# Kernel tuning notes

Measured on AMD Instinct MI355X. Metric: run time of the kernel, lower is better.

## Reference

```python
import jax, jax.numpy as jnp
import numpy as np

TEMPERATURE = 0.07


def setup_inputs() -> dict:
    key = jax.random.key(0)
    k1, k2 = jax.random.split(key)
    B, V, C, H, W = 4, 2, 128, 32, 32
    features = jax.random.normal(k1, (B, V, C, H, W), dtype=jnp.float32)
    # L2-normalize per-pixel feature vectors (channel dim), as contrastive
    # embeddings are in practice; the original exp() is unstabilized.
    features = features / jnp.linalg.norm(features, axis=2, keepdims=True)
    labels = jax.random.randint(k2, (B, V, H, W), 0, 4, dtype=jnp.int32)
    return {"features": features, "labels": labels}


def reference(features, labels):
    B, V, C, H, W = features.shape
    # torch.cat(torch.unbind(features, dim=1), dim=0): views stacked along batch
    cf = jnp.transpose(features, (1, 0, 2, 3, 4)).reshape(B * V, C, H, W)
    # kernels = cf.permute(0,2,3,1).reshape(-1, C, 1, 1); conv2d with 1x1 kernels
    # == pairwise dot products of per-pixel feature vectors.
    X = jnp.transpose(cf, (0, 2, 3, 1)).reshape(-1, C)  # [N, C], N = B*V*H*W
    N = X.shape[0]
    logits = (X @ X.T) / TEMPERATURE  # [N, N]

    lab = jnp.transpose(labels, (1, 0, 2, 3)).reshape(-1)  # [N]
    mask = (lab[:, None] == lab[None, :]).astype(logits.dtype)  # [N, N]
    logits_mask = 1.0 - jnp.eye(N, dtype=logits.dtype)  # zero the diagonal
    mask = mask * logits_mask

    exp_logits = jnp.exp(logits) * logits_mask
    log_prob = logits - jnp.log(jnp.sum(exp_logits, axis=1, keepdims=True))
    mean_log_prob_pos = jnp.sum(mask * log_prob, axis=1) / jnp.sum(mask, axis=1)
    loss = -mean_log_prob_pos  # [N]

    non_bg = (lab != 0).astype(logits.dtype)
    return jnp.sum(loss * non_bg) / jnp.sum(non_bg)
```

## Files before the change

### kernel.cpp

```cpp
#include <hip/hip_runtime.h>
#include <hip/hip_bf16.h>
#include <stdint.h>

typedef short bf16x8 __attribute__((ext_vector_type(8)));
typedef float f32x16 __attribute__((ext_vector_type(16)));

#define NROWS 8192
#define CDIM  128
#define TEMP  0.07f
#define C1F   20.6099291555566248f

#define OFF_S    0
#define OFF_G    32768
#define OFF_HIST (32768 + 2048)
#define OFF_SUM  (32768 + 2048 + 16)
#define OFF_TKT  (32768 + 2048 + 16 + 4)
#define ZBYTES   (32768 + 2048 + 16 + 4 + 4)
#define ZWORDS   (ZBYTES / 4)

__device__ __forceinline__ float bf2f(unsigned short u) {
  union { unsigned int i; float f; } x; x.i = ((unsigned int)u) << 16; return x.f;
}
__device__ __forceinline__ unsigned short f2bf(float f) {
  union { float f; unsigned int i; } x; x.f = f;
  unsigned int r = x.i + 0x7fffu + ((x.i >> 16) & 1u);
  return (unsigned short)(r >> 16);
}
__device__ __forceinline__ float fexp2(float x) {
#if __has_builtin(__builtin_amdgcn_exp2f)
  return __builtin_amdgcn_exp2f(x);
#else
  return exp2f(x);
#endif
}

__global__ __launch_bounds__(256) void k_pack(const float* __restrict__ F,
                                              unsigned short* __restrict__ Xb,
                                              float* __restrict__ zbase) {
  const int tid = threadIdx.x;
  {
    int idx = blockIdx.x * 256 + tid;
    if (idx < ZWORDS) zbase[idx] = 0.0f;
  }
  __shared__ float lds[128 * 33];
  const int g   = blockIdx.x >> 5;
  const int hw0 = (blockIdx.x & 31) << 5;
#pragma unroll
  for (int p = 0; p < 16; ++p) {
    int c  = p * 8 + (tid >> 5);
    int hw = hw0 + (tid & 31);
    lds[c * 33 + (tid & 31)] = F[(g * 128 + c) * 1024 + hw];
  }
  __syncthreads();
#pragma unroll
  for (int p = 0; p < 16; ++p) {
    int hwl = p * 2 + (tid >> 7);
    int c   = tid & 127;
    int row = g * 1024 + hw0 + hwl;
    Xb[row * 128 + c] = f2bf(lds[c * 33 + hwl]);
  }
}

__global__ __launch_bounds__(256, 4) void k_main(const unsigned short* __restrict__ Xb,
                                                 const int* __restrict__ labels,
                                                 float* __restrict__ S,
                                                 float* __restrict__ G,
                                                 int* __restrict__ hist) {
  __shared__ int4 ldsB[2][2][16 * 33];
  const int bid = blockIdx.x;
  const int tid = threadIdx.x;
  const int lane = tid & 63;

  if (bid < 128) {
    const int rchunk = bid >> 3;
    const int cbase  = (bid & 7) * 16;
    const int cl     = tid & 15;
    const int rg     = tid >> 4;
    float a0 = 0.f, a1 = 0.f, a2 = 0.f, a3 = 0.f;
    const int nend = rchunk * 512 + 512;
    for (int n = rchunk * 512 + rg; n < nend; n += 16) {
      int   lab = labels[n];
      float v   = bf2f(Xb[n * 128 + cbase + cl]);
      a0 += (lab == 0) ? v : 0.f;
      a1 += (lab == 1) ? v : 0.f;
      a2 += (lab == 2) ? v : 0.f;
      a3 += (lab == 3) ? v : 0.f;
    }
    a0 += __shfl_xor(a0, 16, 64); a0 += __shfl_xor(a0, 32, 64);
    a1 += __shfl_xor(a1, 16, 64); a1 += __shfl_xor(a1, 32, 64);
    a2 += __shfl_xor(a2, 16, 64); a2 += __shfl_xor(a2, 32, 64);
    a3 += __shfl_xor(a3, 16, 64); a3 += __shfl_xor(a3, 32, 64);
    if (lane < 16) {
      int c = cbase + lane;
      atomicAdd(&G[0 * 128 + c], a0);
      atomicAdd(&G[1 * 128 + c], a1);
      atomicAdd(&G[2 * 128 + c], a2);
      atomicAdd(&G[3 * 128 + c], a3);
    }
    if (bid == 0) {
      int h0 = 0, h1 = 0, h2 = 0, h3 = 0;
      for (int n = tid; n < NROWS; n += 256) {
        int lab = labels[n];
        h0 += (lab == 0); h1 += (lab == 1); h2 += (lab == 2); h3 += (lab == 3);
      }
      for (int mm = 1; mm < 64; mm <<= 1) {
        h0 += __shfl_xor(h0, mm, 64); h1 += __shfl_xor(h1, mm, 64);
        h2 += __shfl_xor(h2, mm, 64); h3 += __shfl_xor(h3, mm, 64);
      }
      if (lane == 0) {
        atomicAdd(&hist[0], h0); atomicAdd(&hist[1], h1);
        atomicAdd(&hist[2], h2); atomicAdd(&hist[3], h3);
      }
    }
    return;
  }

  const int b        = bid - 128;
  const int wave     = tid >> 6;
  const int rowBlock = b >> 4;
  const int split    = b & 15;
  const int r0       = rowBlock * 128 + wave * 32;
  const int col0     = split * 512;
  const int m        = lane & 31;
  const int half     = lane >> 5;

  bf16x8 afrag[8];
#pragma unroll
  for (int s = 0; s < 8; ++s)
    afrag[s] = *(const bf16x8*)(Xb + (r0 + m) * CDIM + (half + 2 * s) * 8);

  float accS[16];
#pragma unroll
  for (int r = 0; r < 16; ++r) accS[r] = 0.f;

  const int n_l = tid >> 3;
  const int bq  = tid & 7;
  const unsigned short* src = Xb + (col0 + n_l) * CDIM + bq * 16;
  int4 v0 = *(const int4*)src;
  int4 v1 = *(const int4*)(src + 8);
  int4 v2 = *(const int4*)(src + 32 * CDIM);
  int4 v3 = *(const int4*)(src + 32 * CDIM + 8);
  ldsB[0][0][(2 * bq) * 33 + n_l]     = v0;
  ldsB[0][0][(2 * bq + 1) * 33 + n_l] = v1;
  ldsB[0][1][(2 * bq) * 33 + n_l]     = v2;
  ldsB[0][1][(2 * bq + 1) * 33 + n_l] = v3;
  src += 64 * CDIM;
  v0 = *(const int4*)src;
  v1 = *(const int4*)(src + 8);
  v2 = *(const int4*)(src + 32 * CDIM);
  v3 = *(const int4*)(src + 32 * CDIM + 8);

  for (int t = 0; t < 8; ++t) {
    __syncthreads();
    if (t < 7) {
      const int nb = (t + 1) & 1;
      ldsB[nb][0][(2 * bq) * 33 + n_l]     = v0;
      ldsB[nb][0][(2 * bq + 1) * 33 + n_l] = v1;
      ldsB[nb][1][(2 * bq) * 33 + n_l]     = v2;
      ldsB[nb][1][(2 * bq + 1) * 33 + n_l] = v3;
    }
    if (t < 6) {
      src += 64 * CDIM;
      v0 = *(const int4*)src;
      v1 = *(const int4*)(src + 8);
      v2 = *(const int4*)(src + 32 * CDIM);
      v3 = *(const int4*)(src + 32 * CDIM + 8);
    }
    const int cur = t & 1;
#pragma unroll
    for (int u = 0; u < 2; ++u) {
      f32x16 acc;
#pragma unroll
      for (int r = 0; r < 16; ++r) acc[r] = 0.f;
#pragma unroll
      for (int s = 0; s < 8; ++s) {
        bf16x8 bfrag = *(const bf16x8*)&ldsB[cur][u][(half + 2 * s) * 33 + m];
        acc = __builtin_amdgcn_mfma_f32_32x32x16_bf16(afrag[s], bfrag, acc, 0, 0, 0);
      }
      const int colbase = col0 + t * 64 + u * 32;
      if (r0 == colbase) {
        const int colg = colbase + m;
#pragma unroll
        for (int r = 0; r < 16; ++r) {
          int   row = r0 + (r & 3) + 8 * (r >> 2) + 4 * half;
          float arg = (row == colg) ? -1e30f : acc[r] * C1F;
          accS[r] += fexp2(arg);
        }
      } else {
#pragma unroll
        for (int r = 0; r < 16; ++r) accS[r] += fexp2(acc[r] * C1F);
      }
    }
  }

#pragma unroll
  for (int r = 0; r < 16; ++r) {
    float v = accS[r];
    v += __shfl_xor(v, 1, 64);
    v += __shfl_xor(v, 2, 64);
    v += __shfl_xor(v, 4, 64);
    v += __shfl_xor(v, 8, 64);
    v += __shfl_xor(v, 16, 64);
    accS[r] = v;
  }
  if (m == 0) {
#pragma unroll
    for (int r = 0; r < 16; ++r) {
      int row = r0 + (r & 3) + 8 * (r >> 2) + 4 * half;
      atomicAdd(&S[row], accS[r]);
    }
  }
}

__global__ __launch_bounds__(256) void k_loss(const unsigned short* __restrict__ Xb,
                                              const int* __restrict__ labels,
                                              const float* __restrict__ S,
                                              const float* __restrict__ G,
                                              const int* __restrict__ hist,
                                              float* __restrict__ sumLoss,
                                              int* __restrict__ ticket,
                                              float* __restrict__ out) {
  const int i   = blockIdx.x * 256 + threadIdx.x;
  const int lab = labels[i];
  const float* g = G + lab * 128;
  const unsigned short* x = Xb + i * CDIM;
  float dot = 0.f, nrm = 0.f;
#pragma unroll
  for (int cc = 0; cc < 16; ++cc) {
    int4 q = *(const int4*)(x + cc * 8);
    const unsigned int* qs = (const unsigned int*)&q;
#pragma unroll
    for (int j = 0; j < 4; ++j) {
      unsigned int u = qs[j];
      float lo = __uint_as_float(u << 16);
      float hi = __uint_as_float(u & 0xffff0000u);
      int   ci = cc * 8 + j * 2;
      dot += lo * g[ci] + hi * g[ci + 1];
      nrm += lo * lo + hi * hi;
    }
  }
  float Si   = S[i];
  float cnt  = (float)(hist[lab] - 1);
  float loss = logf(Si) - (dot - nrm) / (TEMP * cnt);
  float contrib = (lab != 0) ? loss : 0.f;
  for (int mm = 1; mm < 64; mm <<= 1) contrib += __shfl_xor(contrib, mm, 64);
  __shared__ float ws4[4];
  if ((threadIdx.x & 63) == 0) ws4[threadIdx.x >> 6] = contrib;
  __syncthreads();
  if (threadIdx.x == 0) {
    atomicAdd(sumLoss, ws4[0] + ws4[1] + ws4[2] + ws4[3]);
    __threadfence();
    int t = atomicAdd(ticket, 1);
    if (t == 31) {
      float total = atomicAdd(sumLoss, 0.0f);
      out[0] = total / (float)(NROWS - hist[0]);
    }
  }
}

extern "C" void kernel_launch(void* const* d_in, const int* in_sizes, int n_in,
                              void* d_out, int out_size, void* d_ws, size_t ws_size,
                              hipStream_t stream) {
  const float* F      = (const float*)d_in[0];
  const int*   labels = (const int*)d_in[1];
  char* ws = (char*)d_ws;

  unsigned short* Xb      = (unsigned short*)ws;
  const size_t    offS    = (size_t)NROWS * CDIM * 2;
  float*          S       = (float*)(ws + offS + OFF_S);
  float*          G       = (float*)(ws + offS + OFF_G);
  int*            hist    = (int*)(ws + offS + OFF_HIST);
  float*          sumLoss = (float*)(ws + offS + OFF_SUM);
  int*            ticket  = (int*)(ws + offS + OFF_TKT);

  hipLaunchKernelGGL(k_pack, dim3(256), dim3(256), 0, stream, F, Xb, S);
  hipLaunchKernelGGL(k_main, dim3(1152), dim3(256), 0, stream, Xb, labels, S, G, hist);
  hipLaunchKernelGGL(k_loss, dim3(32), dim3(256), 0, stream, Xb, labels, S, G, hist,
                     sumLoss, ticket, (float*)d_out);
}
```

Measured before the change: 100.4 us.

## Double rows per wave in logsumexp GEMM and move class sums into pack

Each wave now computes two 32-row MFMA tiles against every LDS-staged B fragment, so each block covers 256 rows and the grid drops from 1152 to 520 blocks. This halves B-tile loads and LDS traffic per output. The per-class feature sums and label histogram are computed as per-block partials inside the pack kernel from the fp32 LDS tile, then reduced by 8 extra blocks in the main kernel instead of 128 atomic-heavy blocks. The cost is higher register pressure (launch bounds lowered to 2 blocks per SM) and fewer blocks, which reduces parallelism and latency hiding.

```diff
diff --git a/kernel.cpp b/kernel.cpp
--- a/kernel.cpp
+++ b/kernel.cpp
@@ -17,6 +17,8 @@
 #define OFF_TKT  (32768 + 2048 + 16 + 4)
 #define ZBYTES   (32768 + 2048 + 16 + 4 + 4)
 #define ZWORDS   (ZBYTES / 4)
+#define OFF_GPART (ZBYTES + 8)
+#define OFF_CPART (OFF_GPART + 256 * 512 * 4)
 
 __device__ __forceinline__ float bf2f(unsigned short u) {
   union { unsigned int i; float f; } x; x.i = ((unsigned int)u) << 16; return x.f;
@@ -35,16 +37,22 @@
 }
 
 __global__ __launch_bounds__(256) void k_pack(const float* __restrict__ F,
+                                              const int* __restrict__ labels,
                                               unsigned short* __restrict__ Xb,
-                                              float* __restrict__ zbase) {
+                                              float* __restrict__ zbase,
+                                              float* __restrict__ Gpart,
+                                              int* __restrict__ Cpart) {
   const int tid = threadIdx.x;
   {
     int idx = blockIdx.x * 256 + tid;
     if (idx < ZWORDS) zbase[idx] = 0.0f;
   }
   __shared__ float lds[128 * 33];
+  __shared__ int   slab[32];
+  __shared__ float gred[4][128];
   const int g   = blockIdx.x >> 5;
   const int hw0 = (blockIdx.x & 31) << 5;
+  if (tid < 32) slab[tid] = labels[g * 1024 + hw0 + tid];
 #pragma unroll
   for (int p = 0; p < 16; ++p) {
     int c  = p * 8 + (tid >> 5);
@@ -59,79 +67,93 @@
     int row = g * 1024 + hw0 + hwl;
     Xb[row * 128 + c] = f2bf(lds[c * 33 + hwl]);
   }
-}
-
-__global__ __launch_bounds__(256, 4) void k_main(const unsigned short* __restrict__ Xb,
-                                                 const int* __restrict__ labels,
+  const int c  = tid & 127;
+  const int rh = tid >> 7;
+  float a0 = 0.f, a1 = 0.f, a2 = 0.f, a3 = 0.f;
+#pragma unroll
+  for (int k = 0; k < 16; ++k) {
+    int   hwl = rh * 16 + k;
+    float v   = lds[c * 33 + hwl];
+    int   lab = slab[hwl];
+    a0 += (lab == 0) ? v : 0.f;
+    a1 += (lab == 1) ? v : 0.f;
+    a2 += (lab == 2) ? v : 0.f;
+    a3 += (lab == 3) ? v : 0.f;
+  }
+  if (rh == 1) { gred[0][c] = a0; gred[1][c] = a1; gred[2][c] = a2; gred[3][c] = a3; }
+  if (tid >= 32 && tid < 36) {
+    int j = tid - 32, cnt = 0;
+#pragma unroll
+    for (int k2 = 0; k2 < 32; ++k2) cnt += (slab[k2] == j);
+    Cpart[blockIdx.x * 4 + j] = cnt;
+  }
+  __syncthreads();
+  if (rh == 0) {
+    float* gp = Gpart + blockIdx.x * 512;
+    gp[0 * 128 + c] = a0 + gred[0][c];
+    gp[1 * 128 + c] = a1 + gred[1][c];
+    gp[2 * 128 + c] = a2 + gred[2][c];
+    gp[3 * 128 + c] = a3 + gred[3][c];
+  }
+}
+
+__global__ __launch_bounds__(256, 2) void k_main(const unsigned short* __restrict__ Xb,
                                                  float* __restrict__ S,
                                                  float* __restrict__ G,
-                                                 int* __restrict__ hist) {
+                                                 int* __restrict__ hist,
+                                                 const float* __restrict__ Gpart,
+                                                 const int* __restrict__ Cpart) {
   __shared__ int4 ldsB[2][2][16 * 33];
-  const int bid = blockIdx.x;
-  const int tid = threadIdx.x;
+  const int bid  = blockIdx.x;
+  const int tid  = threadIdx.x;
   const int lane = tid & 63;
 
-  if (bid < 128) {
-    const int rchunk = bid >> 3;
-    const int cbase  = (bid & 7) * 16;
-    const int cl     = tid & 15;
-    const int rg     = tid >> 4;
-    float a0 = 0.f, a1 = 0.f, a2 = 0.f, a3 = 0.f;
-    const int nend = rchunk * 512 + 512;
-    for (int n = rchunk * 512 + rg; n < nend; n += 16) {
-      int   lab = labels[n];
-      float v   = bf2f(Xb[n * 128 + cbase + cl]);
-      a0 += (lab == 0) ? v : 0.f;
-      a1 += (lab == 1) ? v : 0.f;
-      a2 += (lab == 2) ? v : 0.f;
-      a3 += (lab == 3) ? v : 0.f;
-    }
-    a0 += __shfl_xor(a0, 16, 64); a0 += __shfl_xor(a0, 32, 64);
-    a1 += __shfl_xor(a1, 16, 64); a1 += __shfl_xor(a1, 32, 64);
-    a2 += __shfl_xor(a2, 16, 64); a2 += __shfl_xor(a2, 32, 64);
-    a3 += __shfl_xor(a3, 16, 64); a3 += __shfl_xor(a3, 32, 64);
-    if (lane < 16) {
-      int c = cbase + lane;
-      atomicAdd(&G[0 * 128 + c], a0);
-      atomicAdd(&G[1 * 128 + c], a1);
-      atomicAdd(&G[2 * 128 + c], a2);
-      atomicAdd(&G[3 * 128 + c], a3);
-    }
-    if (bid == 0) {
-      int h0 = 0, h1 = 0, h2 = 0, h3 = 0;
-      for (int n = tid; n < NROWS; n += 256) {
-        int lab = labels[n];
-        h0 += (lab == 0); h1 += (lab == 1); h2 += (lab == 2); h3 += (lab == 3);
+  if (bid >= 512) {
+    const int rb = bid - 512;
+    const int l  = tid & 63;
+    const int w  = tid >> 6;
+    const float* gp = Gpart + (w * 64) * 512 + rb * 64 + l;
+    float s = 0.f;
+#pragma unroll 8
+    for (int k = 0; k < 64; ++k) s += gp[k * 512];
+    __shared__ float red[4][64];
+    red[w][l] = s;
+    __syncthreads();
+    if (w == 0) G[rb * 64 + l] = red[0][l] + red[1][l] + red[2][l] + red[3][l];
+    if (rb == 0) {
+      int4 c4 = ((const int4*)Cpart)[tid];
+      for (int mm = 1; mm < 64; mm <<= 1) {
+        c4.x += __shfl_xor(c4.x, mm, 64);
+        c4.y += __shfl_xor(c4.y, mm, 64);
+        c4.z += __shfl_xor(c4.z, mm, 64);
+        c4.w += __shfl_xor(c4.w, mm, 64);
       }
-      for (int mm = 1; mm < 64; mm <<= 1) {
-        h0 += __shfl_xor(h0, mm, 64); h1 += __shfl_xor(h1, mm, 64);
-        h2 += __shfl_xor(h2, mm, 64); h3 += __shfl_xor(h3, mm, 64);
-      }
-      if (lane == 0) {
-        atomicAdd(&hist[0], h0); atomicAdd(&hist[1], h1);
-        atomicAdd(&hist[2], h2); atomicAdd(&hist[3], h3);
-      }
+      __shared__ int hred[4][4];
+      if (l == 0) { hred[w][0] = c4.x; hred[w][1] = c4.y; hred[w][2] = c4.z; hred[w][3] = c4.w; }
+      __syncthreads();
+      if (tid < 4) hist[tid] = hred[0][tid] + hred[1][tid] + hred[2][tid] + hred[3][tid];
     }
     return;
   }
 
-  const int b        = bid - 128;
   const int wave     = tid >> 6;
-  const int rowBlock = b >> 4;
-  const int split    = b & 15;
-  const int r0       = rowBlock * 128 + wave * 32;
+  const int rowBlock = bid >> 4;
+  const int split    = bid & 15;
+  const int r0       = rowBlock * 256 + wave * 64;
   const int col0     = split * 512;
   const int m        = lane & 31;
   const int half     = lane >> 5;
 
-  bf16x8 afrag[8];
-#pragma unroll
-  for (int s = 0; s < 8; ++s)
-    afrag[s] = *(const bf16x8*)(Xb + (r0 + m) * CDIM + (half + 2 * s) * 8);
-
-  float accS[16];
-#pragma unroll
-  for (int r = 0; r < 16; ++r) accS[r] = 0.f;
+  bf16x8 afrag0[8], afrag1[8];
+#pragma unroll
+  for (int s = 0; s < 8; ++s) {
+    afrag0[s] = *(const bf16x8*)(Xb + (r0 + m) * CDIM + (half + 2 * s) * 8);
+    afrag1[s] = *(const bf16x8*)(Xb + (r0 + 32 + m) * CDIM + (half + 2 * s) * 8);
+  }
+
+  float accS0[16], accS1[16];
+#pragma unroll
+  for (int r = 0; r < 16; ++r) { accS0[r] = 0.f; accS1[r] = 0.f; }
 
   const int n_l = tid >> 3;
   const int bq  = tid & 7;
@@ -169,13 +191,14 @@
     const int cur = t & 1;
 #pragma unroll
     for (int u = 0; u < 2; ++u) {
-      f32x16 acc;
-#pragma unroll
-      for (int r = 0; r < 16; ++r) acc[r] = 0.f;
+      f32x16 acc0, acc1;
+#pragma unroll
+      for (int r = 0; r < 16; ++r) { acc0[r] = 0.f; acc1[r] = 0.f; }
 #pragma unroll
       for (int s = 0; s < 8; ++s) {
         bf16x8 bfrag = *(const bf16x8*)&ldsB[cur][u][(half + 2 * s) * 33 + m];
-        acc = __builtin_amdgcn_mfma_f32_32x32x16_bf16(afrag[s], bfrag, acc, 0, 0, 0);
+        acc0 = __builtin_amdgcn_mfma_f32_32x32x16_bf16(afrag0[s], bfrag, acc0, 0, 0, 0);
+        acc1 = __builtin_amdgcn_mfma_f32_32x32x16_bf16(afrag1[s], bfrag, acc1, 0, 0, 0);
       }
       const int colbase = col0 + t * 64 + u * 32;
       if (r0 == colbase) {
@@ -183,31 +206,51 @@
 #pragma unroll
         for (int r = 0; r < 16; ++r) {
           int   row = r0 + (r & 3) + 8 * (r >> 2) + 4 * half;
-          float arg = (row == colg) ? -1e30f : acc[r] * C1F;
-          accS[r] += fexp2(arg);
+          float arg = (row == colg) ? -1e30f : acc0[r] * C1F;
+          accS0[r] += fexp2(arg);
         }
       } else {
 #pragma unroll
-        for (int r = 0; r < 16; ++r) accS[r] += fexp2(acc[r] * C1F);
+        for (int r = 0; r < 16; ++r) accS0[r] += fexp2(acc0[r] * C1F);
       }
+      if (r0 + 32 == colbase) {
+        const int colg = colbase + m;
+#pragma unroll
+        for (int r = 0; r < 16; ++r) {
+          int   row = r0 + 32 + (r & 3) + 8 * (r >> 2) + 4 * half;
+          float arg = (row == colg) ? -1e30f : acc1[r] * C1F;
+          accS1[r] += fexp2(arg);
+        }
+      } else {
+#pragma unroll
+        for (int r = 0; r < 16; ++r) accS1[r] += fexp2(acc1[r] * C1F);
+      }
     }
   }
 
 #pragma unroll
   for (int r = 0; r < 16; ++r) {
-    float v = accS[r];
+    float v = accS0[r];
     v += __shfl_xor(v, 1, 64);
     v += __shfl_xor(v, 2, 64);
     v += __shfl_xor(v, 4, 64);
     v += __shfl_xor(v, 8, 64);
     v += __shfl_xor(v, 16, 64);
-    accS[r] = v;
+    accS0[r] = v;
+    float v2 = accS1[r];
+    v2 += __shfl_xor(v2, 1, 64);
+    v2 += __shfl_xor(v2, 2, 64);
+    v2 += __shfl_xor(v2, 4, 64);
+    v2 += __shfl_xor(v2, 8, 64);
+    v2 += __shfl_xor(v2, 16, 64);
+    accS1[r] = v2;
   }
   if (m == 0) {
 #pragma unroll
     for (int r = 0; r < 16; ++r) {
-      int row = r0 + (r & 3) + 8 * (r >> 2) + 4 * half;
-      atomicAdd(&S[row], accS[r]);
+      int rowoff = (r & 3) + 8 * (r >> 2) + 4 * half;
+      atomicAdd(&S[r0 + rowoff], accS0[r]);
+      atomicAdd(&S[r0 + 32 + rowoff], accS1[r]);
     }
   }
 }
@@ -272,9 +315,11 @@
   int*            hist    = (int*)(ws + offS + OFF_HIST);
   float*          sumLoss = (float*)(ws + offS + OFF_SUM);
   int*            ticket  = (int*)(ws + offS + OFF_TKT);
-
-  hipLaunchKernelGGL(k_pack, dim3(256), dim3(256), 0, stream, F, Xb, S);
-  hipLaunchKernelGGL(k_main, dim3(1152), dim3(256), 0, stream, Xb, labels, S, G, hist);
+  float*          Gpart   = (float*)(ws + offS + OFF_GPART);
+  int*            Cpart   = (int*)(ws + offS + OFF_CPART);
+
+  hipLaunchKernelGGL(k_pack, dim3(256), dim3(256), 0, stream, F, labels, Xb, S, Gpart, Cpart);
+  hipLaunchKernelGGL(k_main, dim3(520), dim3(256), 0, stream, Xb, S, G, hist, Gpart, Cpart);
   hipLaunchKernelGGL(k_loss, dim3(32), dim3(256), 0, stream, Xb, labels, S, G, hist,
                      sumLoss, ticket, (float*)d_out);
 }
```

Measured after the change: 93.28 us, median of 2. -7.1%, faster.
